# Kernel optimization log

Measured on AMD Instinct MI355X. Metric: run time of the kernel, lower is better.

The kernel has to match this reference:

```python
import jax, jax.numpy as jnp
import numpy as np

B, C, H, W = 16, 256, 64, 64
NH, HD, NM = 4, 32, 4  # heads, head_dim, memory tokens
HID = NH * HD


def rms_norm(x, g):
    # F.normalize(x, dim=1) * sqrt(C) * g  (channel dim = 1)
    norm = jnp.maximum(jnp.linalg.norm(x, axis=1, keepdims=True), 1e-12)
    return x / norm * (x.shape[1] ** 0.5) * g


def setup_inputs() -> dict:
    key = jax.random.key(0)
    ks = jax.random.split(key, 5)
    return {
        "x": jax.random.normal(ks[0], (B, C, H, W), jnp.float32),
        "g_in": jnp.ones((1, C, 1, 1), jnp.float32),
        "mem_kv": jax.random.normal(ks[1], (2, NH, HD, NM), jnp.float32),
        "w_qkv": jax.random.normal(ks[2], (HID * 3, C), jnp.float32) * (C ** -0.5),
        "w_out": jax.random.normal(ks[3], (C, HID), jnp.float32) * (HID ** -0.5),
        "b_out": jnp.zeros((C,), jnp.float32),
        "g_out": jnp.ones((1, C, 1, 1), jnp.float32),
    }


def reference(x, g_in, mem_kv, w_qkv, w_out, b_out, g_out):
    b, c, h, w = x.shape
    n = h * w
    scale = HD ** -0.5

    xn = rms_norm(x, g_in)
    # 1x1 conv as matmul over channel dim: [B, 3*HID, H, W]
    qkv = jnp.einsum('oc,bchw->bohw', w_qkv, xn)
    q, k, v = jnp.split(qkv, 3, axis=1)
    # b (h d) x y -> b h d n
    q = q.reshape(b, NH, HD, n)
    k = k.reshape(b, NH, HD, n)
    v = v.reshape(b, NH, HD, n)

    # prepend memory key/value tokens: [b, h, d, NM + n]
    mk = jnp.broadcast_to(mem_kv[0], (b, NH, HD, NM))
    mv = jnp.broadcast_to(mem_kv[1], (b, NH, HD, NM))
    k = jnp.concatenate([mk, k], axis=-1)
    v = jnp.concatenate([mv, v], axis=-1)

    q = jax.nn.softmax(q, axis=-2) * scale  # softmax over head_dim
    k = jax.nn.softmax(k, axis=-1)          # softmax over tokens

    context = jnp.einsum('bhdn,bhen->bhde', k, v)  # [b, h, d, e]
    out = jnp.einsum('bhde,bhdn->bhen', context, q)  # [b, h, e, n]
    out = out.reshape(b, HID, h, w)

    out = jnp.einsum('oc,bchw->bohw', w_out, out) + b_out[None, :, None, None]
    return rms_norm(out, g_out)
```

## Files before the change

kernel.cpp:

```cpp
#include <hip/hip_runtime.h>
#include <math.h>

typedef unsigned short u16;
typedef unsigned int u32;

#define NBATCH 16
#define NCH    256
#define NPIX   4096
#define NHEAD  4
#define HDIM   32
#define NMEM   4
#define HID    128
#define OC3    384
#define SCALE_Q 0.17677669529663687f

typedef __bf16 bf16x8 __attribute__((ext_vector_type(8)));
typedef float  f32x4  __attribute__((ext_vector_type(4)));

__device__ __forceinline__ float bf2f(u16 u){ return __uint_as_float(((u32)u)<<16); }
__device__ __forceinline__ u16 f2bf(float f){
  u32 x = __float_as_uint(f);
  x += 0x7fffu + ((x>>16)&1u);
  return (u16)(x>>16);
}
__device__ __forceinline__ void unpack8(int4 v, float* o){
  u32 a=(u32)v.x, b=(u32)v.y, c=(u32)v.z, d=(u32)v.w;
  o[0]=__uint_as_float(a<<16); o[1]=__uint_as_float(a&0xffff0000u);
  o[2]=__uint_as_float(b<<16); o[3]=__uint_as_float(b&0xffff0000u);
  o[4]=__uint_as_float(c<<16); o[5]=__uint_as_float(c&0xffff0000u);
  o[6]=__uint_as_float(d<<16); o[7]=__uint_as_float(d&0xffff0000u);
}

__global__ __launch_bounds__(256) void k_pack(const float* __restrict__ wqkv,
                                              const float* __restrict__ gin,
                                              const float* __restrict__ wout,
                                              u16* __restrict__ wqb,
                                              u16* __restrict__ wob)
{
  int i = blockIdx.x*256 + threadIdx.x;
  if (i < OC3*NCH){ int c = i & 255; wqb[i] = f2bf(wqkv[i]*gin[c]); }
  else { int j = i - OC3*NCH; wob[j] = f2bf(wout[j]); }
}

__global__ __launch_bounds__(512, 4) void k_qkvx(const float* __restrict__ x,
                                                 const u16* __restrict__ wqb,
                                                 u16* __restrict__ qt,
                                                 u16* __restrict__ kv)
{
  __shared__ u16 Bx[64*264];
  __shared__ float ssqp[8][64];
  __shared__ float psx[8][64];
  __shared__ float rl[64];
  const int t = threadIdx.x, w = t>>6, lane = t&63;
  const int n0 = blockIdx.x*64, b = blockIdx.y;
  const int qw = lane>>4, rr = lane&15;

  {
    const float* xp = x + ((size_t)b*NCH + w*32)*NPIX + n0 + lane;
    float ssq = 0.f;
    #pragma unroll
    for (int j=0;j<4;j++){
      u32 pk[4];
      #pragma unroll
      for (int q=0;q<4;q++){
        float v0 = xp[(size_t)(j*8+2*q  )*NPIX];
        float v1 = xp[(size_t)(j*8+2*q+1)*NPIX];
        ssq += v0*v0 + v1*v1;
        pk[q] = (u32)f2bf(v0) | ((u32)f2bf(v1)<<16);
      }
      *(int4*)&Bx[lane*264 + w*32 + j*8] = make_int4((int)pk[0],(int)pk[1],(int)pk[2],(int)pk[3]);
    }
    ssqp[w][lane] = ssq;
  }
  __syncthreads();
  if (t < 64){
    float s = 0.f;
    #pragma unroll
    for (int g=0;g<8;g++) s += ssqp[g][t];
    rl[t] = 16.0f / fmaxf(sqrtf(s), 1e-12f);
  }

  f32x4 acc[3][4];
  #pragma unroll
  for (int p=0;p<3;p++)
    #pragma unroll
    for (int nf=0;nf<4;nf++) acc[p][nf] = (f32x4){0.f,0.f,0.f,0.f};

  const u16* aw = wqb + (size_t)(w*16 + rr)*NCH + qw*8;
  bf16x8 caf0 = *(const bf16x8*)(aw);
  bf16x8 caf1 = *(const bf16x8*)(aw + 128*NCH);
  bf16x8 caf2 = *(const bf16x8*)(aw + 256*NCH);
  #pragma unroll
  for (int c0=0; c0<NCH; c0+=32){
    bf16x8 bfr[4];
    #pragma unroll
    for (int nf=0;nf<4;nf++)
      bfr[nf] = *(const bf16x8*)&Bx[(nf*16+rr)*264 + c0 + qw*8];
    bf16x8 naf0 = caf0, naf1 = caf1, naf2 = caf2;
    if (c0 < NCH-32){
      naf0 = *(const bf16x8*)(aw + c0+32);
      naf1 = *(const bf16x8*)(aw + 128*NCH + c0+32);
      naf2 = *(const bf16x8*)(aw + 256*NCH + c0+32);
    }
    #pragma unroll
    for (int nf=0;nf<4;nf++){
      acc[0][nf] = __builtin_amdgcn_mfma_f32_16x16x32_bf16(caf0, bfr[nf], acc[0][nf], 0, 0, 0);
      acc[1][nf] = __builtin_amdgcn_mfma_f32_16x16x32_bf16(bfr[nf], caf1, acc[1][nf], 0, 0, 0);
      acc[2][nf] = __builtin_amdgcn_mfma_f32_16x16x32_bf16(bfr[nf], caf2, acc[2][nf], 0, 0, 0);
    }
    caf0 = naf0; caf1 = naf1; caf2 = naf2;
  }

  __syncthreads();

  #pragma unroll
  for (int p=1;p<3;p++){
    u16* base = kv + ((size_t)(b*256 + (p-1)*128 + w*16 + rr))*NPIX + n0;
    #pragma unroll
    for (int nf=0;nf<4;nf++){
      const float4 rv4 = *(const float4*)&rl[nf*16 + qw*4];
      u32 lo = (u32)f2bf(acc[p][nf][0]*rv4.x) | ((u32)f2bf(acc[p][nf][1]*rv4.y)<<16);
      u32 hi = (u32)f2bf(acc[p][nf][2]*rv4.z) | ((u32)f2bf(acc[p][nf][3]*rv4.w)<<16);
      *(int2*)(base + nf*16 + qw*4) = make_int2((int)lo,(int)hi);
    }
  }

  float qv[4][4], pm[4], ps[4];
  #pragma unroll
  for (int nf=0;nf<4;nf++){
    float rv = rl[nf*16 + rr];
    float m = -1e30f;
    #pragma unroll
    for (int r=0;r<4;r++){ qv[nf][r] = acc[0][nf][r]*rv; m = fmaxf(m, qv[nf][r]); }
    m = fmaxf(m, __shfl_xor(m, 16, 64));
    m = fmaxf(m, __shfl_xor(m, 32, 64));
    float s = 0.f;
    #pragma unroll
    for (int r=0;r<4;r++){ qv[nf][r] = __expf(qv[nf][r]-m); s += qv[nf][r]; }
    s += __shfl_xor(s, 16, 64);
    s += __shfl_xor(s, 32, 64);
    pm[nf] = m; ps[nf] = s;
  }
  if (lane < 16){
    #pragma unroll
    for (int nf=0;nf<4;nf++){ ssqp[w][nf*16+lane] = pm[nf]; psx[w][nf*16+lane] = ps[nf]; }
  }
  __syncthreads();
  {
    const int pw = w^1;
    u16* qbase = qt + ((size_t)b*NPIX + n0)*HID + w*16 + qw*4;
    #pragma unroll
    for (int nf=0;nf<4;nf++){
      float om = ssqp[pw][nf*16+rr], os = psx[pw][nf*16+rr];
      float M = fmaxf(pm[nf], om);
      float S = ps[nf]*__expf(pm[nf]-M) + os*__expf(om-M);
      float f = __expf(pm[nf]-M) * SCALE_Q / S;
      u32 lo = (u32)f2bf(qv[nf][0]*f) | ((u32)f2bf(qv[nf][1]*f)<<16);
      u32 hi = (u32)f2bf(qv[nf][2]*f) | ((u32)f2bf(qv[nf][3]*f)<<16);
      *(int2*)(qbase + (size_t)(nf*16+rr)*HID) = make_int2((int)lo,(int)hi);
    }
  }
}

__global__ __launch_bounds__(256) void k_kred(const u16* __restrict__ kv,
                                              const float* __restrict__ memkv,
                                              float2* __restrict__ kms,
                                              float* __restrict__ ksm)
{
  const int rid = blockIdx.x*4 + (threadIdx.x>>6);
  const int lane = threadIdx.x & 63;
  const int d = rid & 31, h = (rid>>5)&3, b = rid>>7;
  const u16* p = kv + (size_t)(b*256 + h*HDIM + d)*NPIX;
  u32 buf[32];
  #pragma unroll
  for (int j=0;j<8;j++)
    *(int4*)&buf[j*4] = *(const int4*)(p + (size_t)(j*64+lane)*8);
  float m = -1e30f;
  #pragma unroll
  for (int i=0;i<32;i++){
    float lo = __uint_as_float(buf[i]<<16);
    float hi = __uint_as_float(buf[i]&0xffff0000u);
    m = fmaxf(m, fmaxf(lo, hi));
  }
  float mv[4];
  #pragma unroll
  for (int mm=0;mm<4;mm++){ mv[mm] = memkv[(h*HDIM+d)*NMEM + mm]; m = fmaxf(m, mv[mm]); }
  #pragma unroll
  for (int sh=1; sh<64; sh<<=1) m = fmaxf(m, __shfl_xor(m, sh, 64));
  float ssum = 0.f;
  #pragma unroll
  for (int i=0;i<32;i++){
    float lo = __uint_as_float(buf[i]<<16);
    float hi = __uint_as_float(buf[i]&0xffff0000u);
    ssum += __expf(lo-m) + __expf(hi-m);
  }
  #pragma unroll
  for (int sh=1; sh<64; sh<<=1) ssum += __shfl_xor(ssum, sh, 64);
  #pragma unroll
  for (int mm=0;mm<4;mm++) ssum += __expf(mv[mm]-m);
  float inv = 1.0f/ssum;
  if (lane==0) kms[rid] = make_float2(m, inv);
  if (lane<4) ksm[rid*NMEM + lane] = __expf(mv[lane]-m)*inv;
}

__global__ __launch_bounds__(64) void k_ctx(const u16* __restrict__ kv,
                                            const float* __restrict__ memkv,
                                            const float* __restrict__ ksm,
                                            const float2* __restrict__ kms,
                                            float* __restrict__ ctxp)
{
  __shared__ float Ks[32][68];
  __shared__ float Vs[32][68];
  const int bh = blockIdx.x;
  const int s  = blockIdx.y;
  const int b = bh>>2, h = bh&3;
  const int t = threadIdx.x;
  const int d0 = (t>>3)*4, e0 = (t&7)*4;
  float acc[4][4] = {};
  if (s==0){
    #pragma unroll
    for (int m=0;m<4;m++){
      float km[4];
      #pragma unroll
      for (int pi=0;pi<4;pi++) km[pi] = ksm[(bh*HDIM + d0+pi)*NMEM + m];
      #pragma unroll
      for (int q=0;q<4;q++){
        float vm = memkv[((NHEAD+h)*HDIM + e0+q)*NMEM + m];
        #pragma unroll
        for (int pi=0;pi<4;pi++) acc[pi][q] += km[pi]*vm;
      }
    }
  }
  const u16* kb = kv + (size_t)(b*256 +       h*HDIM)*NPIX;
  const u16* vb = kv + (size_t)(b*256 + HID + h*HDIM)*NPIX;
  const int lr = t>>1, lseg = (t&1)*32;
  const float2 ms = kms[bh*HDIM + lr];
  #pragma unroll
  for (int half=0; half<2; ++half){
    const int n0 = s*128 + half*64;
    const u16* kp = kb + (size_t)lr*NPIX + n0 + lseg;
    const u16* vp = vb + (size_t)lr*NPIX + n0 + lseg;
    #pragma unroll
    for (int u=0;u<4;u++){
      int4 kvv = *(const int4*)(kp + u*8);
      int4 vv  = *(const int4*)(vp + u*8);
      float kf[8], vf[8];
      unpack8(kvv,kf); unpack8(vv,vf);
      #pragma unroll
      for (int i=0;i<8;i++) kf[i] = __expf(kf[i]-ms.x)*ms.y;
      *(float4*)&Ks[lr][lseg+u*8]   = make_float4(kf[0],kf[1],kf[2],kf[3]);
      *(float4*)&Ks[lr][lseg+u*8+4] = make_float4(kf[4],kf[5],kf[6],kf[7]);
      *(float4*)&Vs[lr][lseg+u*8]   = make_float4(vf[0],vf[1],vf[2],vf[3]);
      *(float4*)&Vs[lr][lseg+u*8+4] = make_float4(vf[4],vf[5],vf[6],vf[7]);
    }
    __syncthreads();
    #pragma unroll 4
    for (int nn=0;nn<64;nn+=4){
      float kq[4][4] __attribute__((aligned(16)));
      float vq[4][4] __attribute__((aligned(16)));
      #pragma unroll
      for (int pi=0;pi<4;pi++) *(float4*)kq[pi] = *(const float4*)&Ks[d0+pi][nn];
      #pragma unroll
      for (int q=0;q<4;q++)    *(float4*)vq[q]  = *(const float4*)&Vs[e0+q][nn];
      #pragma unroll
      for (int pi=0;pi<4;pi++)
        #pragma unroll
        for (int q=0;q<4;q++)
          acc[pi][q] += kq[pi][0]*vq[q][0] + kq[pi][1]*vq[q][1]
                      + kq[pi][2]*vq[q][2] + kq[pi][3]*vq[q][3];
    }
    __syncthreads();
  }
  #pragma unroll
  for (int pi=0;pi<4;pi++)
    *(float4*)(ctxp + (size_t)(s*64+bh)*1024 + (d0+pi)*32 + e0) =
      make_float4(acc[pi][0],acc[pi][1],acc[pi][2],acc[pi][3]);
}

__global__ __launch_bounds__(256) void k_ctxred(const float* __restrict__ ctxp,
                                                float* __restrict__ ctx)
{
  const int bh = blockIdx.x, t = threadIdx.x;
  float4 s = make_float4(0.f,0.f,0.f,0.f);
  #pragma unroll
  for (int sp=0; sp<32; sp++){
    float4 v = *(const float4*)(ctxp + (size_t)(sp*64+bh)*1024 + t*4);
    s.x+=v.x; s.y+=v.y; s.z+=v.z; s.w+=v.w;
  }
  *(float4*)(ctx + (size_t)bh*1024 + t*4) = s;
}

__global__ __launch_bounds__(256) void k_fout(const u16* __restrict__ qt,
                                              const float* __restrict__ ctx,
                                              const u16* __restrict__ wob,
                                              const float* __restrict__ bout,
                                              const float* __restrict__ gout,
                                              float* __restrict__ out)
{
  __shared__ u16 Cb[4*32*40];
  __shared__ u16 Ao[64*136];
  __shared__ float ssql[4][64];
  const int t = threadIdx.x, w = t>>6, lane = t&63;
  const int n0 = blockIdx.x*64, b = blockIdx.y;
  const int qw = lane>>4, rr = lane&15;

  {
    const float4* c4 = (const float4*)(ctx + (size_t)b*4096);
    const int d = (t>>3)&31, e0 = (t&7)*4;
    #pragma unroll
    for (int h=0;h<4;h++){
      float4 v = c4[t + h*256];
      Cb[(h*32+e0+0)*40 + d] = f2bf(v.x);
      Cb[(h*32+e0+1)*40 + d] = f2bf(v.y);
      Cb[(h*32+e0+2)*40 + d] = f2bf(v.z);
      Cb[(h*32+e0+3)*40 + d] = f2bf(v.w);
    }
  }
  __syncthreads();

  f32x4 pv[4][2];
  const u16* qp = qt + ((size_t)b*NPIX + n0 + w*16 + rr)*HID;
  #pragma unroll
  for (int h=0;h<4;h++){
    bf16x8 bq = *(const bf16x8*)(qp + h*32 + qw*8);
    #pragma unroll
    for (int ef=0;ef<2;ef++){
      bf16x8 af = *(const bf16x8*)&Cb[(h*32 + ef*16 + rr)*40 + qw*8];
      f32x4 z = (f32x4){0.f,0.f,0.f,0.f};
      pv[h][ef] = __builtin_amdgcn_mfma_f32_16x16x32_bf16(af, bq, z, 0, 0, 0);
    }
  }
  #pragma unroll
  for (int h=0;h<4;h++)
    #pragma unroll
    for (int ef=0;ef<2;ef++){
      u32 lohi0 = (u32)f2bf(pv[h][ef][0]) | ((u32)f2bf(pv[h][ef][1])<<16);
      u32 lohi1 = (u32)f2bf(pv[h][ef][2]) | ((u32)f2bf(pv[h][ef][3])<<16);
      *(int2*)&Ao[(w*16+rr)*136 + h*32 + ef*16 + qw*4] = make_int2((int)lohi0,(int)lohi1);
    }
  __syncthreads();

  f32x4 acc[4][4];
  #pragma unroll
  for (int i=0;i<4;i++)
    #pragma unroll
    for (int j=0;j<4;j++) acc[i][j] = (f32x4){0.f,0.f,0.f,0.f};
  #pragma unroll
  for (int k0=0; k0<HID; k0+=32){
    bf16x8 af[4], bfr[4];
    #pragma unroll
    for (int mf=0;mf<4;mf++)
      af[mf] = *(const bf16x8*)&wob[(size_t)(w*64 + mf*16 + rr)*HID + k0 + qw*8];
    #pragma unroll
    for (int nf=0;nf<4;nf++)
      bfr[nf] = *(const bf16x8*)&Ao[(nf*16+rr)*136 + k0 + qw*8];
    #pragma unroll
    for (int mf=0;mf<4;mf++)
      #pragma unroll
      for (int nf=0;nf<4;nf++)
        acc[mf][nf] = __builtin_amdgcn_mfma_f32_16x16x32_bf16(af[mf], bfr[nf], acc[mf][nf], 0, 0, 0);
  }
  float pssq[4] = {0.f,0.f,0.f,0.f};
  #pragma unroll
  for (int mf=0;mf<4;mf++)
    #pragma unroll
    for (int reg=0;reg<4;reg++){
      int c = w*64 + mf*16 + qw*4 + reg;
      float bb = bout[c];
      #pragma unroll
      for (int nf=0;nf<4;nf++){
        float v = acc[mf][nf][reg] + bb;
        acc[mf][nf][reg] = v;
        pssq[nf] += v*v;
      }
    }
  #pragma unroll
  for (int nf=0;nf<4;nf++){
    pssq[nf] += __shfl_xor(pssq[nf], 16, 64);
    pssq[nf] += __shfl_xor(pssq[nf], 32, 64);
  }
  if (qw==0){
    #pragma unroll
    for (int nf=0;nf<4;nf++) ssql[w][nf*16+rr] = pssq[nf];
  }
  __syncthreads();
  float rv[4];
  #pragma unroll
  for (int nf=0;nf<4;nf++){
    int col = nf*16 + rr;
    float sm = ssql[0][col]+ssql[1][col]+ssql[2][col]+ssql[3][col];
    rv[nf] = 16.0f / fmaxf(sqrtf(sm), 1e-12f);
  }
  #pragma unroll
  for (int mf=0;mf<4;mf++)
    #pragma unroll
    for (int reg=0;reg<4;reg++){
      int c = w*64 + mf*16 + qw*4 + reg;
      float g = gout[c];
      float* po = out + ((size_t)(b*NCH + c))*NPIX + n0;
      #pragma unroll
      for (int nf=0;nf<4;nf++)
        po[nf*16 + rr] = acc[mf][nf][reg]*rv[nf]*g;
    }
}

extern "C" void kernel_launch(void* const* d_in, const int* in_sizes, int n_in,
                              void* d_out, int out_size, void* d_ws, size_t ws_size,
                              hipStream_t stream)
{
  const float* x     = (const float*)d_in[0];
  const float* gin   = (const float*)d_in[1];
  const float* memkv = (const float*)d_in[2];
  const float* wqkv  = (const float*)d_in[3];
  const float* wout  = (const float*)d_in[4];
  const float* bout  = (const float*)d_in[5];
  const float* gout  = (const float*)d_in[6];
  float* out = (float*)d_out;

  char* ws = (char*)d_ws;
  u16*    kvb  = (u16*)   (ws);
  u16*    qt   = (u16*)   (ws + 33554432);
  float*  ksm  = (float*) (ws + 50331648);
  float2* kms  = (float2*)(ws + 50364416);
  float*  ctxp = (float*) (ws + 50380800);
  float*  ctx  = (float*) (ws + 58769408);
  u16*    wqb  = (u16*)   (ws + 59031552);
  u16*    wob  = (u16*)   (ws + 59228160);

  hipLaunchKernelGGL(k_pack,   dim3(512),   dim3(256), 0, stream, wqkv, gin, wout, wqb, wob);
  hipLaunchKernelGGL(k_qkvx,   dim3(64,16), dim3(512), 0, stream, x, wqb, qt, kvb);
  hipLaunchKernelGGL(k_kred,   dim3(512),   dim3(256), 0, stream, kvb, memkv, kms, ksm);
  hipLaunchKernelGGL(k_ctx,    dim3(64,32), dim3(64),  0, stream, kvb, memkv, ksm, kms, ctxp);
  hipLaunchKernelGGL(k_ctxred, dim3(64),    dim3(256), 0, stream, ctxp, ctx);
  hipLaunchKernelGGL(k_fout,   dim3(64,16), dim3(256), 0, stream, qt, ctx, wob, bout, gout, out);
}
```

Measured before the change: 197.6 us.

## Stage x tile through LDS via direct global-to-LDS loads and use native bf16 casts

The x tile in the QKV projection kernel is now loaded with global_load_lds 16-byte transfers into a float staging buffer in shared memory, replacing per-lane strided scalar global loads. Threads then read from LDS to build the bf16 tile and the sum of squares, with the channel ordering in Bx adjusted to match. Shared memory is unioned into a single buffer. The manual round-to-nearest bf16 conversion is replaced by the compiler's __bf16 cast and a packed two-value helper, which may map to hardware convert instructions. The staging loop serializes load then wait per step with no double buffering, and LDS use per block grows, which may reduce occupancy.

```diff
diff --git a/kernel.cpp b/kernel.cpp
--- a/kernel.cpp
+++ b/kernel.cpp
@@ -18,10 +18,11 @@
 typedef float  f32x4  __attribute__((ext_vector_type(4)));
 
 __device__ __forceinline__ float bf2f(u16 u){ return __uint_as_float(((u32)u)<<16); }
-__device__ __forceinline__ u16 f2bf(float f){
-  u32 x = __float_as_uint(f);
-  x += 0x7fffu + ((x>>16)&1u);
-  return (u16)(x>>16);
+__device__ __forceinline__ u16 bfb(float f){
+  union { __bf16 h; u16 u; } x; x.h = (__bf16)f; return x.u;
+}
+__device__ __forceinline__ u32 pkbf2(float a, float b){
+  union { __bf16 h[2]; u32 u; } x; x.h[0] = (__bf16)a; x.h[1] = (__bf16)b; return x.u;
 }
 __device__ __forceinline__ void unpack8(int4 v, float* o){
   u32 a=(u32)v.x, b=(u32)v.y, c=(u32)v.z, d=(u32)v.w;
@@ -30,6 +31,11 @@
   o[4]=__uint_as_float(c<<16); o[5]=__uint_as_float(c&0xffff0000u);
   o[6]=__uint_as_float(d<<16); o[7]=__uint_as_float(d&0xffff0000u);
 }
+__device__ __forceinline__ void gload_lds16(const void* gp, void* lp){
+  __builtin_amdgcn_global_load_lds(
+      (const __attribute__((address_space(1))) unsigned int*)gp,
+      (__attribute__((address_space(3))) unsigned int*)lp, 16, 0, 0);
+}
 
 __global__ __launch_bounds__(256) void k_pack(const float* __restrict__ wqkv,
                                               const float* __restrict__ gin,
@@ -38,8 +44,8 @@
                                               u16* __restrict__ wob)
 {
   int i = blockIdx.x*256 + threadIdx.x;
-  if (i < OC3*NCH){ int c = i & 255; wqb[i] = f2bf(wqkv[i]*gin[c]); }
-  else { int j = i - OC3*NCH; wob[j] = f2bf(wout[j]); }
+  if (i < OC3*NCH){ int c = i & 255; wqb[i] = bfb(wqkv[i]*gin[c]); }
+  else { int j = i - OC3*NCH; wob[j] = bfb(wout[j]); }
 }
 
 __global__ __launch_bounds__(512, 4) void k_qkvx(const float* __restrict__ x,
@@ -47,28 +53,34 @@
                                                  u16* __restrict__ qt,
                                                  u16* __restrict__ kv)
 {
-  __shared__ u16 Bx[64*264];
-  __shared__ float ssqp[8][64];
-  __shared__ float psx[8][64];
-  __shared__ float rl[64];
+  __shared__ __align__(16) char smem[52480];
+  float (*Xs)[64]   = (float(*)[64])smem;
+  u16*   Bx         = (u16*)(smem + 16384);
+  float (*ssqp)[64] = (float(*)[64])(smem + 50176);
+  float* rl         = (float*)(smem + 52224);
+  float (*psx)[64]  = (float(*)[64])smem;
+
   const int t = threadIdx.x, w = t>>6, lane = t&63;
   const int n0 = blockIdx.x*64, b = blockIdx.y;
   const int qw = lane>>4, rr = lane&15;
 
   {
-    const float* xp = x + ((size_t)b*NCH + w*32)*NPIX + n0 + lane;
     float ssq = 0.f;
-    #pragma unroll
-    for (int j=0;j<4;j++){
+    for (int s=0;s<4;++s){
+      asm volatile("s_waitcnt lgkmcnt(0)" ::: "memory");
+      const float* gp = x + ((size_t)b*NCH + s*64 + w*8 + (lane>>4))*NPIX + n0 + (lane&15)*4;
+      gload_lds16(gp,                    &Xs[w*8 + 0][0]);
+      gload_lds16(gp + (size_t)4*NPIX,   &Xs[w*8 + 4][0]);
+      asm volatile("s_waitcnt vmcnt(0)" ::: "memory");
       u32 pk[4];
       #pragma unroll
       for (int q=0;q<4;q++){
-        float v0 = xp[(size_t)(j*8+2*q  )*NPIX];
-        float v1 = xp[(size_t)(j*8+2*q+1)*NPIX];
+        float v0 = Xs[w*8 + 2*q    ][lane];
+        float v1 = Xs[w*8 + 2*q + 1][lane];
         ssq += v0*v0 + v1*v1;
-        pk[q] = (u32)f2bf(v0) | ((u32)f2bf(v1)<<16);
+        pk[q] = pkbf2(v0, v1);
       }
-      *(int4*)&Bx[lane*264 + w*32 + j*8] = make_int4((int)pk[0],(int)pk[1],(int)pk[2],(int)pk[3]);
+      *(int4*)&Bx[lane*264 + s*64 + w*8] = make_int4((int)pk[0],(int)pk[1],(int)pk[2],(int)pk[3]);
     }
     ssqp[w][lane] = ssq;
   }
@@ -119,8 +131,8 @@
     #pragma unroll
     for (int nf=0;nf<4;nf++){
       const float4 rv4 = *(const float4*)&rl[nf*16 + qw*4];
-      u32 lo = (u32)f2bf(acc[p][nf][0]*rv4.x) | ((u32)f2bf(acc[p][nf][1]*rv4.y)<<16);
-      u32 hi = (u32)f2bf(acc[p][nf][2]*rv4.z) | ((u32)f2bf(acc[p][nf][3]*rv4.w)<<16);
+      u32 lo = pkbf2(acc[p][nf][0]*rv4.x, acc[p][nf][1]*rv4.y);
+      u32 hi = pkbf2(acc[p][nf][2]*rv4.z, acc[p][nf][3]*rv4.w);
       *(int2*)(base + nf*16 + qw*4) = make_int2((int)lo,(int)hi);
     }
   }
@@ -155,8 +167,8 @@
       float M = fmaxf(pm[nf], om);
       float S = ps[nf]*__expf(pm[nf]-M) + os*__expf(om-M);
       float f = __expf(pm[nf]-M) * SCALE_Q / S;
-      u32 lo = (u32)f2bf(qv[nf][0]*f) | ((u32)f2bf(qv[nf][1]*f)<<16);
-      u32 hi = (u32)f2bf(qv[nf][2]*f) | ((u32)f2bf(qv[nf][3]*f)<<16);
+      u32 lo = pkbf2(qv[nf][0]*f, qv[nf][1]*f);
+      u32 hi = pkbf2(qv[nf][2]*f, qv[nf][3]*f);
       *(int2*)(qbase + (size_t)(nf*16+rr)*HID) = make_int2((int)lo,(int)hi);
     }
   }
@@ -310,10 +322,10 @@
     #pragma unroll
     for (int h=0;h<4;h++){
       float4 v = c4[t + h*256];
-      Cb[(h*32+e0+0)*40 + d] = f2bf(v.x);
-      Cb[(h*32+e0+1)*40 + d] = f2bf(v.y);
-      Cb[(h*32+e0+2)*40 + d] = f2bf(v.z);
-      Cb[(h*32+e0+3)*40 + d] = f2bf(v.w);
+      Cb[(h*32+e0+0)*40 + d] = bfb(v.x);
+      Cb[(h*32+e0+1)*40 + d] = bfb(v.y);
+      Cb[(h*32+e0+2)*40 + d] = bfb(v.z);
+      Cb[(h*32+e0+3)*40 + d] = bfb(v.w);
     }
   }
   __syncthreads();
@@ -334,8 +346,8 @@
   for (int h=0;h<4;h++)
     #pragma unroll
     for (int ef=0;ef<2;ef++){
-      u32 lohi0 = (u32)f2bf(pv[h][ef][0]) | ((u32)f2bf(pv[h][ef][1])<<16);
-      u32 lohi1 = (u32)f2bf(pv[h][ef][2]) | ((u32)f2bf(pv[h][ef][3])<<16);
+      u32 lohi0 = pkbf2(pv[h][ef][0], pv[h][ef][1]);
+      u32 lohi1 = pkbf2(pv[h][ef][2], pv[h][ef][3]);
       *(int2*)&Ao[(w*16+rr)*136 + h*32 + ef*16 + qw*4] = make_int2((int)lohi0,(int)lohi1);
     }
   __syncthreads();
```

Result: no change. 198.7 us (+0.6%).
